# Performance work log

Hardware: AMD Instinct MI355X
Metric: run time of the kernel (lower is better)

## Reference

```python
import jax, jax.numpy as jnp
import numpy as np

WZ, WH, WW = 2, 6, 12
N = WZ * WH * WW            # 144 tokens per window
DIM, HEADS = 384, 12
HD = DIM // HEADS           # 32
TOW = (8 // WZ) * (48 // WH)  # type_of_windows = 32
NW = 96 // WW               # longitude windows = 8
B_ = 1 * TOW * NW           # 256
TABLE = (2 * WW - 1) * WH * WH * WZ * WZ  # 3312


def _position_index():
    zi = np.arange(WZ); zj = -np.arange(WZ) * WZ
    hi = np.arange(WH); hj = -np.arange(WH) * WH
    w = np.arange(WW)
    c1 = np.stack(np.meshgrid(zi, hi, w, indexing='ij')).reshape(3, -1)
    c2 = np.stack(np.meshgrid(zj, hj, w, indexing='ij')).reshape(3, -1)
    coords = (c1[:, :, None] - c2[:, None, :]).transpose(1, 2, 0)  # (N, N, 3)
    coords[:, :, 2] += WW - 1
    coords[:, :, 1] *= 2 * WW - 1
    coords[:, :, 0] *= (2 * WW - 1) * WH * WH
    return coords.sum(-1).reshape(-1).astype(np.int32)  # (N*N,)


def setup_inputs() -> dict:
    key = jax.random.key(0)
    ks = jax.random.split(key, 7)
    x = jax.random.normal(ks[0], (B_, N, DIM), dtype=jnp.float32)
    mask = jax.random.normal(ks[1], (NW, N, N), dtype=jnp.float32)
    w_qkv = jax.random.normal(ks[2], (DIM, 3 * DIM), dtype=jnp.float32) * 0.02
    b_qkv = jax.random.normal(ks[3], (3 * DIM,), dtype=jnp.float32) * 0.02
    w_out = jax.random.normal(ks[4], (DIM, DIM), dtype=jnp.float32) * 0.02
    b_out = jax.random.normal(ks[5], (DIM,), dtype=jnp.float32) * 0.02
    bias_table = jax.random.normal(ks[6], (TABLE, TOW, HEADS), dtype=jnp.float32) * 0.02
    position_index = jnp.asarray(_position_index())
    return {"x": x, "mask": mask, "w_qkv": w_qkv, "b_qkv": b_qkv,
            "w_out": w_out, "b_out": b_out, "bias_table": bias_table,
            "position_index": position_index}


def reference(x, mask, w_qkv, b_qkv, w_out, b_out, bias_table, position_index):
    Bw, n, C = x.shape
    scale = HD ** -0.5
    qkv = (x @ w_qkv + b_qkv).reshape(Bw, n, 3, HEADS, HD)
    qkv = jnp.transpose(qkv, (2, 0, 3, 1, 4))  # (3, Bw, H, N, hd)
    q, k, v = qkv[0] * scale, qkv[1], qkv[2]
    attn = jnp.einsum('bhnd,bhmd->bhnm', q, k)  # (Bw, H, N, N)
    # Earth-specific bias: gather table rows by position index, tiled per window group
    r = Bw // TOW
    bias = bias_table[jnp.tile(position_index, r)]          # (r*N*N, TOW, H)
    bias = bias.reshape(n, n, -1, HEADS)                    # (N, N, Bw, H)
    bias = jnp.transpose(bias, (2, 3, 0, 1))                # (Bw, H, N, N)
    attn = attn + bias
    nW = mask.shape[0]
    attn = attn.reshape(Bw // nW, nW, HEADS, n, n) + mask[None, :, None]
    attn = jax.nn.softmax(attn.reshape(Bw, HEADS, n, n), axis=-1)
    out = jnp.einsum('bhnm,bhmd->bhnd', attn, v)            # (Bw, H, N, hd)
    out = jnp.transpose(out, (0, 2, 1, 3)).reshape(Bw, n, C)
    return out @ w_out + b_out
```

## Files before the change

### kernel.cpp

```cpp
#include <hip/hip_runtime.h>
#include <hip/hip_fp16.h>
#include <cstdint>
#include <cstddef>

#define NQQ  (144*144)
#define SCALE 0.17677669529663687f

#define AOH   0ull
#define X16H  0ull
#define QH    14155776ull
#define KH    28311552ull
#define VH    42467328ull
#define WTH   56623104ull
#define WOTH  57065472ull
#define MASKH 57212928ull
#define BIASH 57378816ull
#define WS_NEED_BYTES ((BIASH + 3072ull * 2592ull) * 2ull)

typedef _Float16 half8  __attribute__((ext_vector_type(8)));
typedef _Float16 half4v __attribute__((ext_vector_type(4)));
typedef float    f32x4  __attribute__((ext_vector_type(4)));

typedef __attribute__((address_space(1))) const unsigned int guint;
typedef __attribute__((address_space(3))) unsigned int luint;
#define GLD16(g, l) __builtin_amdgcn_global_load_lds((guint*)(g), (luint*)(l), 16, 0, 0)

__launch_bounds__(256)
__global__ void k_prep(const float* __restrict__ X, _Float16* __restrict__ X16,
                       const float* __restrict__ Wq, _Float16* __restrict__ WqT,
                       const float* __restrict__ Wo, _Float16* __restrict__ WoT,
                       const float* __restrict__ M, _Float16* __restrict__ M16,
                       const float* __restrict__ table, const int* __restrict__ pidx,
                       _Float16* __restrict__ biasOut) {
    __shared__ __align__(16) char psm[13888];
    const int bid = blockIdx.x;
    const int t   = threadIdx.x;
    if (bid < 13824) {
        size_t i = (size_t)bid * 256 + t;
        float4 f = *(const float4*)&X[i * 4];
        _Float16 h[4] = {(_Float16)f.x, (_Float16)f.y, (_Float16)f.z, (_Float16)f.w};
        *(ushort4*)&X16[i * 4] = *(ushort4*)h;
        return;
    }
    if (bid >= 14130) {
        _Float16 (*sTb)[18] = (_Float16(*)[18])psm;
        int* rowsL = (int*)(psm + 13824);
        const int j      = bid - 14130;
        const int s_tile = j / 162;
        const int chunk  = j - s_tile * 162;
        const int i0     = chunk * 16;
        if (t < 16) rowsL[t] = pidx[8 * (i0 + t) + s_tile];
        __syncthreads();
#pragma unroll
        for (int rr = 0; rr < 16; ++rr) {
            int row = rowsL[rr];
            sTb[t][rr] = (_Float16)table[(size_t)row * 384 + t];
            if (t < 128) sTb[t + 256][rr] = (_Float16)table[(size_t)row * 384 + t + 256];
        }
        __syncthreads();
        unsigned int* ob = (unsigned int*)biasOut;
#pragma unroll
        for (int v = t; v < 3072; v += 256) {
            int i1h = v >> 3, dw = v & 7;
            ob[(size_t)(s_tile * 384 + i1h) * 1296 + chunk * 8 + dw] =
                *(const unsigned int*)&sTb[i1h][dw * 2];
        }
        return;
    }
    if (bid >= 13968) {
        size_t i = (size_t)(bid - 13968) * 256 + t;
        float4 f = *(const float4*)&M[i * 4];
        _Float16 h[4] = {(_Float16)f.x, (_Float16)f.y, (_Float16)f.z, (_Float16)f.w};
        *(ushort4*)&M16[i * 4] = *(ushort4*)h;
        return;
    }
    _Float16 (*sT)[72] = (_Float16(*)[72])psm;
    const float* W; _Float16* WT; int K, Cn, cb, kb;
    if (bid < 13932) {
        int j = bid - 13824;
        W = Wq; WT = WqT; K = 384; Cn = 1152;
        cb = (j % 18) * 64; kb = (j / 18) * 64;
    } else {
        int j = bid - 13932;
        W = Wo; WT = WoT; K = 384; Cn = 384;
        cb = (j % 6) * 64; kb = (j / 6) * 64;
    }
#pragma unroll
    for (int i = 0; i < 16; ++i) {
        int id = t + 256 * i;
        int kl = id >> 6, cl = id & 63;
        sT[cl][kl] = (_Float16)W[(size_t)(kb + kl) * Cn + cb + cl];
    }
    __syncthreads();
#pragma unroll
    for (int i = 0; i < 16; ++i) {
        int id = t + 256 * i;
        int cl = id >> 6, kl = id & 63;
        WT[(size_t)(cb + cl) * K + kb + kl] = sT[cl][kl];
    }
}

__launch_bounds__(256)
__global__ void k_qkv_gemm_mfma(const _Float16* __restrict__ X16,
                                const _Float16* __restrict__ WT,
                                const float* __restrict__ bq,
                                _Float16* __restrict__ ws16) {
    __shared__ __align__(16) _Float16 sA[128 * 64];
    __shared__ __align__(16) _Float16 sB[128 * 64];
    const int t    = threadIdx.x;
    const int lane = t & 63;
    const int w    = t >> 6;
    const int quad = lane >> 4;
    const int l15  = lane & 15;
    const int bid = blockIdx.x;
    const int wg  = (bid & 7) * 324 + (bid >> 3);
    const int cy  = wg % 9, rx = wg / 9;
    const int r0  = rx * 128, c0 = cy * 128;
    const int wr  = (w >> 1) * 64, wc = (w & 1) * 64;

    const int drow = t >> 3;
    const int schk = (t & 7) ^ (drow & 7);
    const _Float16* gA = &X16[(size_t)(r0 + drow) * 384 + schk * 8];
    const _Float16* gB = &WT [(size_t)(c0 + drow) * 384 + schk * 8];
    char* lA = (char*)sA + t * 16;
    char* lB = (char*)sB + t * 16;

    const int x7 = l15 & 7;
    const char* rA = (const char*)sA + (wr + l15) * 128;
    const char* rB = (const char*)sB + (wc + l15) * 128;

    f32x4 acc[4][4] = {};

    for (int kk = 0; kk < 384; kk += 64) {
#pragma unroll
        for (int j = 0; j < 4; ++j) {
            GLD16(gA + (size_t)j * 12288 + kk, lA + j * 4096);
            GLD16(gB + (size_t)j * 12288 + kk, lB + j * 4096);
        }
        __syncthreads();
#pragma unroll
        for (int s = 0; s < 2; ++s) {
            const int ca = (((s * 4 + quad) ^ x7) << 4);
            half8 a[4], b[4];
#pragma unroll
            for (int i = 0; i < 4; ++i) a[i] = *(const half8*)(rA + i * 2048 + ca);
#pragma unroll
            for (int j = 0; j < 4; ++j) b[j] = *(const half8*)(rB + j * 2048 + ca);
#pragma unroll
            for (int i = 0; i < 4; ++i)
#pragma unroll
                for (int j = 0; j < 4; ++j)
                    acc[i][j] = __builtin_amdgcn_mfma_f32_16x16x32_f16(a[i], b[j], acc[i][j], 0, 0, 0);
        }
        __syncthreads();
    }

#pragma unroll
    for (int j = 0; j < 4; ++j) {
        int c  = c0 + wc + 16 * j + l15;
        int p  = c / 384;
        int hh = (c >> 5) % 12;
        int d0 = c & 31;
        float bias = bq[c];
        float sc   = (p == 0) ? SCALE : 1.0f;
        size_t base = (p == 0) ? QH : ((p == 1) ? KH : VH);
#pragma unroll
        for (int i = 0; i < 4; ++i) {
#pragma unroll
            for (int reg = 0; reg < 4; ++reg) {
                int r  = r0 + wr + 16 * i + quad * 4 + reg;
                int bw = r / 144;
                int n  = r - bw * 144;
                ws16[base + (((size_t)bw * 12 + hh) * 144 + n) * 32 + d0] =
                    (_Float16)((acc[i][j][reg] + bias) * sc);
            }
        }
    }
}

__launch_bounds__(576)
__global__ void k_attn_fused_mfma(const _Float16* __restrict__ ws16,
                                  const _Float16* __restrict__ mask16,
                                  const float* __restrict__ table,
                                  const int* __restrict__ pidx,
                                  const _Float16* __restrict__ bias_pre,
                                  _Float16* __restrict__ AO) {
    __shared__ __align__(16) char smem[27616];
    _Float16 (*sK)[40]   = (_Float16(*)[40])(smem);
    _Float16 (*sVT)[168] = (_Float16(*)[168])(smem + 11520);
    _Float16* sBias      = (_Float16*)(smem + 22272);

    const int bh = blockIdx.x;
    const int b  = bh / 12;
    const int h  = bh - b * 12;
    const int t  = threadIdx.x;
    const int w    = t >> 6;
    const int lane = t & 63;
    const int quad = lane >> 4;
    const int l15  = lane & 15;

    const int s_tile = b >> 5;
    const int i1     = b & 31;

    const _Float16* qg = ws16 + QH + (size_t)bh * 4608;
    const _Float16* kg = ws16 + KH + (size_t)bh * 4608;
    const _Float16* vg = ws16 + VH + (size_t)bh * 4608;

    half8 aq = *(const half8*)&qg[(size_t)(16 * w + l15) * 32 + quad * 8];

    {
        int row = t >> 2, ko = (t & 3) * 8;
        *(uint4*)&sK[row][ko] = *(const uint4*)&kg[row * 32 + ko];
    }
    for (int i = t; i < 2304; i += 576) {
        unsigned int u = ((const unsigned int*)vg)[i];
        int m  = i >> 4, d0 = (i & 15) * 2;
        int mp = m ^ ((d0 >> 3) << 3);
        sVT[d0][mp]     = ((const _Float16*)&u)[0];
        sVT[d0 + 1][mp] = ((const _Float16*)&u)[1];
    }
    if (t < 512) {
        int d = t & 31, m = 144 + (t >> 5);
        sVT[d][m ^ ((d >> 3) << 3)] = (_Float16)0;
    }
    if (bias_pre) {
        const _Float16* bg = bias_pre + (size_t)bh * 2592;
        for (int i2 = t; i2 < 648; i2 += 576) {
            uint2 wv = *(const uint2*)&bg[i2 * 4];
            int r18 = i2 / 36;
            int col = i2 * 4 - r18 * 144;
            *(uint2*)&sBias[r18 * 148 + col] = wv;
        }
    } else {
        for (int i = t; i < 2592; i += 576) {
            int row = pidx[8 * i + s_tile];
            int r18 = i / 144;
            sBias[r18 * 148 + (i - r18 * 144)] =
                (_Float16)table[(size_t)row * 384 + i1 * 12 + h];
        }
    }
    __syncthreads();

    f32x4 tj[9] = {};
#pragma unroll
    for (int j = 0; j < 9; ++j) {
        half8 bk = *(const half8*)&sK[16 * j + l15][quad * 8];
        tj[j] = __builtin_amdgcn_mfma_f32_16x16x32_f16(bk, aq, tj[j], 0, 0, 0);
    }

    const int q    = 16 * w + l15;
    const int nb18 = q % 18;
    const _Float16* mrow = mask16 + (size_t)(b & 7) * NQQ + (size_t)q * 144 + 4 * quad;
    uint2 mz[9];
#pragma unroll
    for (int j = 0; j < 9; ++j) mz[j] = *(const uint2*)&mrow[16 * j];
#pragma unroll
    for (int j = 0; j < 9; ++j) {
        uint2 bz = *(const uint2*)&sBias[nb18 * 148 + 16 * j + 4 * quad];
        const _Float16* bb = (const _Float16*)&bz;
        const _Float16* mm = (const _Float16*)&mz[j];
#pragma unroll
        for (int reg = 0; reg < 4; ++reg)
            tj[j][reg] += (float)bb[reg] + (float)mm[reg];
    }
    float rmax = tj[0][0];
#pragma unroll
    for (int j = 0; j < 9; ++j)
#pragma unroll
        for (int reg = 0; reg < 4; ++reg) rmax = fmaxf(rmax, tj[j][reg]);
    rmax = fmaxf(rmax, __shfl_xor(rmax, 16));
    rmax = fmaxf(rmax, __shfl_xor(rmax, 32));
    float rsum = 0.0f;
#pragma unroll
    for (int j = 0; j < 9; ++j)
#pragma unroll
        for (int reg = 0; reg < 4; ++reg) {
            tj[j][reg] = __expf(tj[j][reg] - rmax);
            rsum += tj[j][reg];
        }
    rsum += __shfl_xor(rsum, 16);
    rsum += __shfl_xor(rsum, 32);
    const float inv = 1.0f / rsum;

    unsigned int pkA[10], pkB[10];
    pkA[9] = 0u; pkB[9] = 0u;
#pragma unroll
    for (int j = 0; j < 9; ++j) {
        auto a2 = __builtin_amdgcn_cvt_pkrtz(tj[j][0] * inv, tj[j][1] * inv);
        auto b2 = __builtin_amdgcn_cvt_pkrtz(tj[j][2] * inv, tj[j][3] * inv);
        pkA[j] = *(unsigned int*)&a2;
        pkB[j] = *(unsigned int*)&b2;
    }

    const int src_lo = 32 * (quad & 1) + l15;
    const int src_hi = src_lo + 16;
    const bool selhi = (quad >> 1) != 0;
    f32x4 o[2] = {};
#pragma unroll
    for (int kt = 0; kt < 5; ++kt) {
        const int j0 = 2 * kt, j1 = 2 * kt + 1;
        unsigned int a0l = __shfl((int)pkA[j0], src_lo);
        unsigned int a1l = __shfl((int)pkA[j1], src_lo);
        unsigned int b0l = __shfl((int)pkB[j0], src_lo);
        unsigned int b1l = __shfl((int)pkB[j1], src_lo);
        unsigned int a0h = __shfl((int)pkA[j0], src_hi);
        unsigned int a1h = __shfl((int)pkA[j1], src_hi);
        unsigned int b0h = __shfl((int)pkB[j0], src_hi);
        unsigned int b1h = __shfl((int)pkB[j1], src_hi);
        union { uint4 u4; half8 h8; } bp;
        bp.u4.x = selhi ? a1l : a0l;
        bp.u4.y = selhi ? b1l : b0l;
        bp.u4.z = selhi ? a1h : a0h;
        bp.u4.w = selhi ? b1h : b0h;
#pragma unroll
        for (int dt = 0; dt < 2; ++dt) {
            const int vrow = dt * 16 + l15;
            half8 av = *(const half8*)&sVT[vrow][(kt * 32 + quad * 8) ^ ((vrow >> 3) << 3)];
            o[dt] = __builtin_amdgcn_mfma_f32_16x16x32_f16(av, bp.h8, o[dt], 0, 0, 0);
        }
    }

#pragma unroll
    for (int dt = 0; dt < 2; ++dt) {
        int d = dt * 16 + quad * 4;
        half4v hv;
#pragma unroll
        for (int reg = 0; reg < 4; ++reg) hv[reg] = (_Float16)o[dt][reg];
        *(half4v*)&AO[((size_t)b * 144 + q) * 384 + h * 32 + d] = hv;
    }
}

__launch_bounds__(256)
__global__ void k_out_gemm_mfma(const _Float16* __restrict__ A16,
                                const _Float16* __restrict__ WoT,
                                const float* __restrict__ bo,
                                float* __restrict__ out) {
    __shared__ __align__(16) _Float16 sA[128 * 64];
    __shared__ __align__(16) _Float16 sB[128 * 64];
    const int t    = threadIdx.x;
    const int lane = t & 63;
    const int w    = t >> 6;
    const int quad = lane >> 4;
    const int l15  = lane & 15;
    const int bid = blockIdx.x;
    const int wg  = (bid & 7) * 108 + (bid >> 3);
    const int cy  = wg % 3, rx = wg / 3;
    const int r0  = rx * 128, c0 = cy * 128;
    const int wr  = (w >> 1) * 64, wc = (w & 1) * 64;

    const int drow = t >> 3;
    const int schk = (t & 7) ^ (drow & 7);
    const _Float16* gA = &A16[(size_t)(r0 + drow) * 384 + schk * 8];
    const _Float16* gB = &WoT[(size_t)(c0 + drow) * 384 + schk * 8];
    char* lA = (char*)sA + t * 16;
    char* lB = (char*)sB + t * 16;

    const int x7 = l15 & 7;
    const char* rA = (const char*)sA + (wr + l15) * 128;
    const char* rB = (const char*)sB + (wc + l15) * 128;

    f32x4 acc[4][4] = {};

    for (int kk = 0; kk < 384; kk += 64) {
#pragma unroll
        for (int j = 0; j < 4; ++j) {
            GLD16(gA + (size_t)j * 12288 + kk, lA + j * 4096);
            GLD16(gB + (size_t)j * 12288 + kk, lB + j * 4096);
        }
        __syncthreads();
#pragma unroll
        for (int s = 0; s < 2; ++s) {
            const int ca = (((s * 4 + quad) ^ x7) << 4);
            half8 a[4], b[4];
#pragma unroll
            for (int i = 0; i < 4; ++i) a[i] = *(const half8*)(rA + i * 2048 + ca);
#pragma unroll
            for (int j = 0; j < 4; ++j) b[j] = *(const half8*)(rB + j * 2048 + ca);
#pragma unroll
            for (int i = 0; i < 4; ++i)
#pragma unroll
                for (int j = 0; j < 4; ++j)
                    acc[i][j] = __builtin_amdgcn_mfma_f32_16x16x32_f16(a[i], b[j], acc[i][j], 0, 0, 0);
        }
        __syncthreads();
    }

#pragma unroll
    for (int j = 0; j < 4; ++j) {
        int c = c0 + wc + 16 * j + l15;
        float bias = bo[c];
#pragma unroll
        for (int i = 0; i < 4; ++i) {
#pragma unroll
            for (int reg = 0; reg < 4; ++reg) {
                int r = r0 + wr + 16 * i + quad * 4 + reg;
                out[(size_t)r * 384 + c] = acc[i][j][reg] + bias;
            }
        }
    }
}

extern "C" void kernel_launch(void* const* d_in, const int* in_sizes, int n_in,
                              void* d_out, int out_size, void* d_ws, size_t ws_size,
                              hipStream_t stream) {
    const float* x      = (const float*)d_in[0];
    const float* mask   = (const float*)d_in[1];
    const float* w_qkv  = (const float*)d_in[2];
    const float* b_qkv  = (const float*)d_in[3];
    const float* w_out  = (const float*)d_in[4];
    const float* b_out  = (const float*)d_in[5];
    const float* table  = (const float*)d_in[6];
    const int*   pidx   = (const int*)d_in[7];
    float* out = (float*)d_out;
    _Float16* ws16 = (_Float16*)d_ws;

    const bool pre = ws_size >= (size_t)WS_NEED_BYTES;
    _Float16* bias16 = pre ? (ws16 + BIASH) : (_Float16*)nullptr;

    hipLaunchKernelGGL(k_prep,          dim3(pre ? 15426 : 14130), dim3(256), 0, stream,
                       x, ws16 + X16H, w_qkv, ws16 + WTH, w_out, ws16 + WOTH,
                       mask, ws16 + MASKH, table, pidx, bias16);
    hipLaunchKernelGGL(k_qkv_gemm_mfma, dim3(2592), dim3(256), 0, stream,
                       ws16 + X16H, ws16 + WTH, b_qkv, ws16);
    hipLaunchKernelGGL(k_attn_fused_mfma, dim3(3072), dim3(576), 0, stream,
                       ws16, ws16 + MASKH, table, pidx, bias16, ws16 + AOH);
    hipLaunchKernelGGL(k_out_gemm_mfma, dim3(864), dim3(256), 0, stream,
                       ws16 + AOH, ws16 + WOTH, b_out, out);
}
```

Baseline: 257.9 us.

## Double-buffer LDS K-slices in QKV and output GEMMs to overlap loads with MFMA

Both projection GEMMs now split each 64-wide K tile into two 32-wide halves held in ping-pong LDS buffers. The next half is issued with async global-to-LDS loads while MFMAs run on the current half, and the LDS swizzle is redone for 64-byte rows. The aim is to hide global load latency that the old load-sync-compute loop exposed. The cost is twice as many barriers per K step and a new swizzle pattern that could cause bank conflicts if it is wrong.

```diff
diff --git a/kernel.cpp b/kernel.cpp
--- a/kernel.cpp
+++ b/kernel.cpp
@@ -100,13 +100,32 @@
     }
 }
 
+#define STAGE2(dA, dB, kk) do {                                   \
+    GLD16(gA + (kk),          (char*)(dA) + t * 16);              \
+    GLD16(gA + (kk) + 24576,  (char*)(dA) + t * 16 + 4096);       \
+    GLD16(gB + (kk),          (char*)(dB) + t * 16);              \
+    GLD16(gB + (kk) + 24576,  (char*)(dB) + t * 16 + 4096);       \
+} while (0)
+
+#define CSTEP(pA, pB) do {                                        \
+    half8 a[4], b[4];                                             \
+    _Pragma("unroll")                                             \
+    for (int i = 0; i < 4; ++i) a[i] = *(const half8*)((pA) + i * 1024); \
+    _Pragma("unroll")                                             \
+    for (int j = 0; j < 4; ++j) b[j] = *(const half8*)((pB) + j * 1024); \
+    _Pragma("unroll")                                             \
+    for (int i = 0; i < 4; ++i)                                   \
+    _Pragma("unroll")                                             \
+        for (int j = 0; j < 4; ++j)                               \
+            acc[i][j] = __builtin_amdgcn_mfma_f32_16x16x32_f16(a[i], b[j], acc[i][j], 0, 0, 0); \
+} while (0)
+
 __launch_bounds__(256)
 __global__ void k_qkv_gemm_mfma(const _Float16* __restrict__ X16,
                                 const _Float16* __restrict__ WT,
                                 const float* __restrict__ bq,
                                 _Float16* __restrict__ ws16) {
-    __shared__ __align__(16) _Float16 sA[128 * 64];
-    __shared__ __align__(16) _Float16 sB[128 * 64];
+    __shared__ __align__(16) _Float16 sA0[4096], sB0[4096], sA1[4096], sB1[4096];
     const int t    = threadIdx.x;
     const int lane = t & 63;
     const int w    = t >> 6;
@@ -118,40 +137,28 @@
     const int r0  = rx * 128, c0 = cy * 128;
     const int wr  = (w >> 1) * 64, wc = (w & 1) * 64;
 
-    const int drow = t >> 3;
-    const int schk = (t & 7) ^ (drow & 7);
-    const _Float16* gA = &X16[(size_t)(r0 + drow) * 384 + schk * 8];
-    const _Float16* gB = &WT [(size_t)(c0 + drow) * 384 + schk * 8];
-    char* lA = (char*)sA + t * 16;
-    char* lB = (char*)sB + t * 16;
-
-    const int x7 = l15 & 7;
-    const char* rA = (const char*)sA + (wr + l15) * 128;
-    const char* rB = (const char*)sB + (wc + l15) * 128;
+    const int srow = t >> 2;
+    const int skch = (t & 3) ^ ((t >> 3) & 3);
+    const _Float16* gA = &X16[(size_t)(r0 + srow) * 384 + skch * 8];
+    const _Float16* gB = &WT [(size_t)(c0 + srow) * 384 + skch * 8];
+
+    const int swz16 = (quad ^ ((l15 >> 1) & 3)) * 16;
+    const char* rA0 = (const char*)sA0 + (wr + l15) * 64 + swz16;
+    const char* rA1 = (const char*)sA1 + (wr + l15) * 64 + swz16;
+    const char* rB0 = (const char*)sB0 + (wc + l15) * 64 + swz16;
+    const char* rB1 = (const char*)sB1 + (wc + l15) * 64 + swz16;
 
     f32x4 acc[4][4] = {};
 
-    for (int kk = 0; kk < 384; kk += 64) {
-#pragma unroll
-        for (int j = 0; j < 4; ++j) {
-            GLD16(gA + (size_t)j * 12288 + kk, lA + j * 4096);
-            GLD16(gB + (size_t)j * 12288 + kk, lB + j * 4096);
-        }
-        __syncthreads();
-#pragma unroll
-        for (int s = 0; s < 2; ++s) {
-            const int ca = (((s * 4 + quad) ^ x7) << 4);
-            half8 a[4], b[4];
-#pragma unroll
-            for (int i = 0; i < 4; ++i) a[i] = *(const half8*)(rA + i * 2048 + ca);
-#pragma unroll
-            for (int j = 0; j < 4; ++j) b[j] = *(const half8*)(rB + j * 2048 + ca);
-#pragma unroll
-            for (int i = 0; i < 4; ++i)
-#pragma unroll
-                for (int j = 0; j < 4; ++j)
-                    acc[i][j] = __builtin_amdgcn_mfma_f32_16x16x32_f16(a[i], b[j], acc[i][j], 0, 0, 0);
-        }
+    STAGE2(sA0, sB0, 0);
+    __syncthreads();
+#pragma unroll
+    for (int s2 = 0; s2 < 6; ++s2) {
+        STAGE2(sA1, sB1, 64 * s2 + 32);
+        CSTEP(rA0, rB0);
+        __syncthreads();
+        if (s2 < 5) STAGE2(sA0, sB0, 64 * s2 + 64);
+        CSTEP(rA1, rB1);
         __syncthreads();
     }
 
@@ -335,8 +342,7 @@
                                 const _Float16* __restrict__ WoT,
                                 const float* __restrict__ bo,
                                 float* __restrict__ out) {
-    __shared__ __align__(16) _Float16 sA[128 * 64];
-    __shared__ __align__(16) _Float16 sB[128 * 64];
+    __shared__ __align__(16) _Float16 sA0[4096], sB0[4096], sA1[4096], sB1[4096];
     const int t    = threadIdx.x;
     const int lane = t & 63;
     const int w    = t >> 6;
@@ -348,40 +354,28 @@
     const int r0  = rx * 128, c0 = cy * 128;
     const int wr  = (w >> 1) * 64, wc = (w & 1) * 64;
 
-    const int drow = t >> 3;
-    const int schk = (t & 7) ^ (drow & 7);
-    const _Float16* gA = &A16[(size_t)(r0 + drow) * 384 + schk * 8];
-    const _Float16* gB = &WoT[(size_t)(c0 + drow) * 384 + schk * 8];
-    char* lA = (char*)sA + t * 16;
-    char* lB = (char*)sB + t * 16;
-
-    const int x7 = l15 & 7;
-    const char* rA = (const char*)sA + (wr + l15) * 128;
-    const char* rB = (const char*)sB + (wc + l15) * 128;
+    const int srow = t >> 2;
+    const int skch = (t & 3) ^ ((t >> 3) & 3);
+    const _Float16* gA = &A16[(size_t)(r0 + srow) * 384 + skch * 8];
+    const _Float16* gB = &WoT[(size_t)(c0 + srow) * 384 + skch * 8];
+
+    const int swz16 = (quad ^ ((l15 >> 1) & 3)) * 16;
+    const char* rA0 = (const char*)sA0 + (wr + l15) * 64 + swz16;
+    const char* rA1 = (const char*)sA1 + (wr + l15) * 64 + swz16;
+    const char* rB0 = (const char*)sB0 + (wc + l15) * 64 + swz16;
+    const char* rB1 = (const char*)sB1 + (wc + l15) * 64 + swz16;
 
     f32x4 acc[4][4] = {};
 
-    for (int kk = 0; kk < 384; kk += 64) {
-#pragma unroll
-        for (int j = 0; j < 4; ++j) {
-            GLD16(gA + (size_t)j * 12288 + kk, lA + j * 4096);
-            GLD16(gB + (size_t)j * 12288 + kk, lB + j * 4096);
-        }
-        __syncthreads();
-#pragma unroll
-        for (int s = 0; s < 2; ++s) {
-            const int ca = (((s * 4 + quad) ^ x7) << 4);
-            half8 a[4], b[4];
-#pragma unroll
-            for (int i = 0; i < 4; ++i) a[i] = *(const half8*)(rA + i * 2048 + ca);
-#pragma unroll
-            for (int j = 0; j < 4; ++j) b[j] = *(const half8*)(rB + j * 2048 + ca);
-#pragma unroll
-            for (int i = 0; i < 4; ++i)
-#pragma unroll
-                for (int j = 0; j < 4; ++j)
-                    acc[i][j] = __builtin_amdgcn_mfma_f32_16x16x32_f16(a[i], b[j], acc[i][j], 0, 0, 0);
-        }
+    STAGE2(sA0, sB0, 0);
+    __syncthreads();
+#pragma unroll
+    for (int s2 = 0; s2 < 6; ++s2) {
+        STAGE2(sA1, sB1, 64 * s2 + 32);
+        CSTEP(rA0, rB0);
+        __syncthreads();
+        if (s2 < 5) STAGE2(sA0, sB0, 64 * s2 + 64);
+        CSTEP(rA1, rB1);
         __syncthreads();
     }
 
```

New measurement: 267.4 us. 3.7% more time.
